# Kernel optimization log

Measured on AMD Instinct MI355X. Metric: run time of the kernel, lower is better.

## Reference

```python
import jax, jax.numpy as jnp
import numpy as np

L = 64        # label_size = len(label2id)
START = 62    # label2id['START']
STOP = 63     # label2id['STOP']
T = 200000    # sequence length
NEG = -10000.0


def setup_inputs() -> dict:
    key = jax.random.key(0)
    k1, k2 = jax.random.split(key)
    lstm_feats = jax.random.normal(k1, (1, T, L), dtype=jnp.float32)
    transitions = jax.random.normal(k2, (L, L), dtype=jnp.float32)
    # CRF constructor masks: cannot transition INTO START, cannot transition FROM STOP
    transitions = transitions.at[START, :].set(NEG).at[:, STOP].set(NEG)
    return {"lstm_feats": lstm_feats, "transitions": transitions}


def reference(lstm_feats, transitions):
    # Viterbi decode, vectorized over tags; lax.scan over time replaces the
    # nested Python loops of the original (same recurrence, same math).
    feats = lstm_feats[0]  # (T, L)
    init = jnp.full((L,), NEG, dtype=lstm_feats.dtype).at[START].set(0.0)

    def step(v, feat):
        # scores[next, prev] = v[prev] + transitions[next, prev]
        scores = v[None, :] + transitions          # (L, L)
        bp = jnp.argmax(scores, axis=1).astype(jnp.int32)  # backpointers per next_tag
        v_new = jnp.max(scores, axis=1) + feat     # viterbi vars + emission
        return v_new, bp

    v, bptrs = jax.lax.scan(step, init, feats)     # bptrs: (T, L)

    terminal = v + transitions[STOP]               # (L,)
    best = jnp.argmax(terminal).astype(jnp.int32)
    path_score = terminal[best]

    # Backtrack: reverse scan emits the tag chosen at each time step, in order.
    def back(tag, bp):
        return bp[tag], tag

    _, best_path = jax.lax.scan(back, best, bptrs, reverse=True)  # (T,) int32
    return path_score, best_path
```

## Files before the change

kernel.cpp:

```cpp
#include <hip/hip_runtime.h>

#define L 64
#define TLEN 200000
#define CH 528
#define NCH 379
#define LASTLEN (TLEN - (NCH - 1) * CH)
#define NEGV -10000.0f
#define STARTT 62
#define STOPT 63

#define CKPT_OFF 0
#define M_OFF ((NCH + 1) * L * 4)
#define ETAG_OFF (M_OFF + NCH * L)

typedef float f32x4 __attribute__((ext_vector_type(4)));

#define FAST_BARRIER() __asm__ volatile("s_barrier" ::: "memory")
#define STEP_BARRIER() __asm__ volatile("" ::: "memory")

__device__ __forceinline__ float max3f(float a, float b, float c) {
    float r;
    __asm__("v_max3_f32 %0, %1, %2, %3" : "=v"(r) : "v"(a), "v"(b), "v"(c));
    return r;
}

#define RL(v, k) __int_as_float(__builtin_amdgcn_readlane(__float_as_int(v), k))

__global__ __launch_bounds__(256, 1) void k_forward(const float* __restrict__ feats,
                                                    const float* __restrict__ trans,
                                                    float* __restrict__ ckpt) {
    const int tid = threadIdx.x;
    const int l = tid & 63;
    const int w = tid >> 6;
    const int n = l;
    const int pcol = 16 * w + (l & 15);
    const int wswz = (w + (n >> 2)) & 3;

    const f32x4* t4 = reinterpret_cast<const f32x4*>(trans) + n * 16 + w * 4;
    f32x4 q0 = t4[0], q1 = t4[1], q2 = t4[2], q3 = t4[3];
    __asm__ volatile("" : "+v"(q0), "+v"(q1), "+v"(q2), "+v"(q3));

    __shared__ __align__(16) float pm[2][L][4];

    float vcomb = (pcol == STARTT) ? 0.0f : NEGV;

    float fc[8];
#pragma unroll
    for (int j = 0; j < 8; ++j) fc[j] = feats[j * L + pcol];

    int nextck = 0, cidx = 0;

#define FWD_STEP(BUF, FEAT)                                                    \
    do {                                                                       \
                         \
        const float s0 = RL(vcomb, 0),  s1 = RL(vcomb, 1);                     \
        const float s2 = RL(vcomb, 2),  s3 = RL(vcomb, 3);                     \
        const float s4 = RL(vcomb, 4),  s5 = RL(vcomb, 5);                     \
        const float s6 = RL(vcomb, 6),  s7 = RL(vcomb, 7);                     \
        const float s8 = RL(vcomb, 8),  s9 = RL(vcomb, 9);                     \
        const float s10 = RL(vcomb, 10), s11 = RL(vcomb, 11);                  \
        const float s12 = RL(vcomb, 12), s13 = RL(vcomb, 13);                  \
        const float s14 = RL(vcomb, 14), s15 = RL(vcomb, 15);                  \
                     \
        const float c0 = s0 + q0.x,  c1 = s1 + q0.y;                           \
        const float c2 = s2 + q0.z,  c3 = s3 + q0.w;                           \
        const float c4 = s4 + q1.x,  c5 = s5 + q1.y;                           \
        const float c6 = s6 + q1.z,  c7 = s7 + q1.w;                           \
        const float c8 = s8 + q2.x,  c9 = s9 + q2.y;                           \
        const float c10 = s10 + q2.z, c11 = s11 + q2.w;                        \
        const float c12 = s12 + q3.x, c13 = s13 + q3.y;                        \
        const float c14 = s14 + q3.z, c15 = s15 + q3.w;                        \
        const float a0 = max3f(c0, c1, c2);                                    \
        const float a1 = max3f(c3, c4, c5);                                    \
        const float a2 = max3f(c6, c7, c8);                                    \
        const float a3 = max3f(c9, c10, c11);                                  \
        const float a4 = max3f(c12, c13, c14);                                 \
        const float pmv = fmaxf(max3f(a0, a1, a2), max3f(a3, a4, c15));        \
                                       \
        pm[BUF][n][wswz] = pmv;                                                \
        FAST_BARRIER();                                                        \
                       \
        const f32x4 pq = *reinterpret_cast<const f32x4*>(&pm[BUF][pcol][0]);   \
        vcomb = fmaxf(max3f(pq.x, pq.y, pq.z), pq.w) + (FEAT);                 \
    } while (0)

    for (int tb = 0; tb < TLEN; tb += 8) {
        if (tb == nextck) {
            if (l < 16) ckpt[cidx * L + 16 * w + l] = vcomb;
            nextck += CH;
            ++cidx;
        }
        float fn_[8];
        const bool more = (tb + 8) < TLEN;
        if (more) {
#pragma unroll
            for (int j = 0; j < 8; ++j) fn_[j] = feats[(tb + 8 + j) * L + pcol];
        }
        FWD_STEP(0, fc[0]);
        FWD_STEP(1, fc[1]);
        FWD_STEP(0, fc[2]);
        FWD_STEP(1, fc[3]);
        FWD_STEP(0, fc[4]);
        FWD_STEP(1, fc[5]);
        FWD_STEP(0, fc[6]);
        FWD_STEP(1, fc[7]);
        if (more) {
#pragma unroll
            for (int j = 0; j < 8; ++j) fc[j] = fn_[j];
        }
    }
    if (l < 16) ckpt[NCH * L + 16 * w + l] = vcomb;
#undef FWD_STEP
}

__device__ __forceinline__ void load_trow(const float* __restrict__ trans, int n, float* trow) {
#pragma unroll
    for (int i = 0; i < 16; ++i) {
        const f32x4 q = reinterpret_cast<const f32x4*>(trans)[n * 16 + i];
        trow[4 * i + 0] = q.x;
        trow[4 * i + 1] = q.y;
        trow[4 * i + 2] = q.z;
        trow[4 * i + 3] = q.w;
    }
}

__device__ __forceinline__ void replay_chunk(const float* __restrict__ feats,
                                             const float* __restrict__ ckpt,
                                             const float* trow, float* vsh,
                                             unsigned char* bpl, int c, int len, int n) {
    float vreg = ckpt[c * L + n];
    vsh[n] = vreg;
    STEP_BARRIER();
    const int base = c * CH;

    float fc[8];
#pragma unroll
    for (int j = 0; j < 8; ++j) fc[j] = feats[(base + j) * L + n];

    for (int sb = 0; sb < len; sb += 8) {
        float fn_[8];
        const bool more = (sb + 8) < len;
        if (more) {
#pragma unroll
            for (int j = 0; j < 8; ++j) fn_[j] = feats[(base + sb + 8 + j) * L + n];
        }
#pragma unroll
        for (int j = 0; j < 8; ++j) {
            float mc[4];
            int ic[4];
#pragma unroll
            for (int g = 0; g < 4; ++g) {
                float m = -INFINITY;
                int idx = g * 16;
#pragma unroll
                for (int r = 0; r < 4; ++r) {
                    const int pb = g * 16 + r * 4;
                    const f32x4 vv = *reinterpret_cast<const f32x4*>(vsh + pb);
                    const float a = vv.x + trow[pb + 0];
                    const float b = vv.y + trow[pb + 1];
                    const float cc = vv.z + trow[pb + 2];
                    const float d = vv.w + trow[pb + 3];
                    if (a > m)  { m = a;  idx = pb + 0; }
                    if (b > m)  { m = b;  idx = pb + 1; }
                    if (cc > m) { m = cc; idx = pb + 2; }
                    if (d > m)  { m = d;  idx = pb + 3; }
                }
                mc[g] = m;
                ic[g] = idx;
            }
            float m = mc[0];
            int idx = ic[0];
            if (mc[1] > m) { m = mc[1]; idx = ic[1]; }
            if (mc[2] > m) { m = mc[2]; idx = ic[2]; }
            if (mc[3] > m) { m = mc[3]; idx = ic[3]; }

            vreg = m + fc[j];
            bpl[(sb + j) * L + n] = (unsigned char)idx;
            vsh[n] = vreg;
            STEP_BARRIER();
        }
        if (more) {
#pragma unroll
            for (int j = 0; j < 8; ++j) fc[j] = fn_[j];
        }
    }
}

__global__ __launch_bounds__(64, 1) void k_maps(const float* __restrict__ feats,
                                                const float* __restrict__ trans,
                                                const float* __restrict__ ckpt,
                                                unsigned char* __restrict__ M) {
    const int c = blockIdx.x;
    const int n = threadIdx.x;
    const int len = (c == NCH - 1) ? LASTLEN : CH;

    __shared__ __align__(16) float vsh[L];
    __shared__ unsigned char bpl[CH * L];

    float trow[L];
    load_trow(trans, n, trow);
    replay_chunk(feats, ckpt, trow, vsh, bpl, c, len, n);
    __syncthreads();

    int tag = n;
    for (int s = len - 1; s >= 0; --s) tag = bpl[s * L + tag];
    M[c * L + n] = (unsigned char)tag;
}

__global__ __launch_bounds__(64, 1) void k_stitch(const float* __restrict__ trans,
                                                  const float* __restrict__ ckpt,
                                                  const unsigned char* __restrict__ M,
                                                  int* __restrict__ etag,
                                                  float* __restrict__ out) {
    const int n = threadIdx.x;
    __shared__ float tsh[L];
    __shared__ int bsh;
    __shared__ __align__(16) unsigned char msh[NCH * L];

    tsh[n] = ckpt[NCH * L + n] + trans[STOPT * L + n];
    __syncthreads();
    if (n == 0) {
        float m = tsh[0];
        int b = 0;
        for (int p = 1; p < L; ++p)
            if (tsh[p] > m) { m = tsh[p]; b = p; }
        out[0] = m;
        bsh = b;
    }
    __syncthreads();

    for (int i = n; i < (NCH * L) / 4; i += L)
        reinterpret_cast<int*>(msh)[i] = reinterpret_cast<const int*>(M)[i];
    __syncthreads();

    if (n == 0) {
        int carry = bsh;
        for (int c = NCH - 1; c >= 1; --c) {
            etag[c] = carry;
            carry = msh[c * L + carry];
        }
        etag[0] = carry;
    }
}

__global__ __launch_bounds__(64, 1) void k_emit(const float* __restrict__ feats,
                                                const float* __restrict__ trans,
                                                const float* __restrict__ ckpt,
                                                const int* __restrict__ etag,
                                                float* __restrict__ out) {
    const int c = blockIdx.x;
    const int n = threadIdx.x;
    const int len = (c == NCH - 1) ? LASTLEN : CH;

    __shared__ __align__(16) float vsh[L];
    __shared__ unsigned char bpl[CH * L];
    __shared__ unsigned char plc[CH];

    float trow[L];
    load_trow(trans, n, trow);
    replay_chunk(feats, ckpt, trow, vsh, bpl, c, len, n);
    __syncthreads();

    int tag = etag[c];
    for (int s = len - 1; s >= 0; --s) {
        if (n == 0) plc[s] = (unsigned char)tag;
        tag = bpl[s * L + tag];
    }
    __syncthreads();

    for (int i = n; i < len; i += L)
        out[1 + c * CH + i] = (float)plc[i];
}

extern "C" void kernel_launch(void* const* d_in, const int* in_sizes, int n_in,
                              void* d_out, int out_size, void* d_ws, size_t ws_size,
                              hipStream_t stream) {
    const float* feats = (const float*)d_in[0];
    const float* trans = (const float*)d_in[1];
    float* out = (float*)d_out;
    char* ws = (char*)d_ws;
    float* ckpt = (float*)(ws + CKPT_OFF);
    unsigned char* M = (unsigned char*)(ws + M_OFF);
    int* etag = (int*)(ws + ETAG_OFF);

    hipLaunchKernelGGL(k_forward, dim3(1), dim3(256), 0, stream, feats, trans, ckpt);
    hipLaunchKernelGGL(k_maps, dim3(NCH), dim3(64), 0, stream, feats, trans, ckpt, M);
    hipLaunchKernelGGL(k_stitch, dim3(1), dim3(64), 0, stream, trans, ckpt, M, etag, out);
    hipLaunchKernelGGL(k_emit, dim3(NCH), dim3(64), 0, stream, feats, trans, ckpt, etag, out);
}
```

Before: 36.67 ms.

## Repartition forward Viterbi step: quad lanes per tag with LDS broadcast and DPP reduction

Each forward step used to pull 16 previous scores out of the wave with scalar readlanes, reduce partial maxima, exchange the partials through LDS and finish the reduction after the barrier. Now each quad of lanes owns one next-tag and reads the previous score vector from a double-buffered LDS array with vector loads. It reduces its 16-column slices, combines the quad with two DPP permutes, and writes the new score back before the barrier. This removes the serialized readlane chain from the per-step critical path. In exchange it adds wide LDS reads and DPP hazards on every step, and keeps a barrier with no explicit wait after the LDS write.

```diff
diff --git a/kernel.cpp b/kernel.cpp
--- a/kernel.cpp
+++ b/kernel.cpp
@@ -15,6 +15,7 @@
 
 typedef float f32x4 __attribute__((ext_vector_type(4)));
 
+#define WAVE_BARRIER() __asm__ volatile("s_waitcnt lgkmcnt(0)\ns_barrier" ::: "memory")
 #define FAST_BARRIER() __asm__ volatile("s_barrier" ::: "memory")
 #define STEP_BARRIER() __asm__ volatile("" ::: "memory")
 
@@ -24,7 +25,9 @@
     return r;
 }
 
-#define RL(v, k) __int_as_float(__builtin_amdgcn_readlane(__float_as_int(v), k))
+#define QPERM(x, ctrl)                                                         \
+    __int_as_float(__builtin_amdgcn_update_dpp(                                \
+        __float_as_int(x), __float_as_int(x), ctrl, 0xf, 0xf, false))
 
 __global__ __launch_bounds__(256, 1) void k_forward(const float* __restrict__ feats,
                                                     const float* __restrict__ trans,
@@ -32,61 +35,48 @@
     const int tid = threadIdx.x;
     const int l = tid & 63;
     const int w = tid >> 6;
-    const int n = l;
-    const int pcol = 16 * w + (l & 15);
-    const int wswz = (w + (n >> 2)) & 3;
-
-    const f32x4* t4 = reinterpret_cast<const f32x4*>(trans) + n * 16 + w * 4;
+    const int d = 16 * w + (l >> 2);
+    const int g = l & 3;
+    const bool writer = (g == 0);
+
+    const f32x4* t4 = reinterpret_cast<const f32x4*>(trans) + d * 16 + g * 4;
     f32x4 q0 = t4[0], q1 = t4[1], q2 = t4[2], q3 = t4[3];
     __asm__ volatile("" : "+v"(q0), "+v"(q1), "+v"(q2), "+v"(q3));
 
-    __shared__ __align__(16) float pm[2][L][4];
-
-    float vcomb = (pcol == STARTT) ? 0.0f : NEGV;
+    __shared__ __align__(16) float vbuf[2][L];
+
+    float vq = (d == STARTT) ? 0.0f : NEGV;
+    if (writer) vbuf[0][d] = vq;
+    WAVE_BARRIER();
 
     float fc[8];
 #pragma unroll
-    for (int j = 0; j < 8; ++j) fc[j] = feats[j * L + pcol];
+    for (int j = 0; j < 8; ++j) fc[j] = feats[j * L + d];
 
     int nextck = 0, cidx = 0;
 
-#define FWD_STEP(BUF, FEAT)                                                    \
+#define FWD_STEP(RD, WR, FEAT)                                                 \
     do {                                                                       \
-                         \
-        const float s0 = RL(vcomb, 0),  s1 = RL(vcomb, 1);                     \
-        const float s2 = RL(vcomb, 2),  s3 = RL(vcomb, 3);                     \
-        const float s4 = RL(vcomb, 4),  s5 = RL(vcomb, 5);                     \
-        const float s6 = RL(vcomb, 6),  s7 = RL(vcomb, 7);                     \
-        const float s8 = RL(vcomb, 8),  s9 = RL(vcomb, 9);                     \
-        const float s10 = RL(vcomb, 10), s11 = RL(vcomb, 11);                  \
-        const float s12 = RL(vcomb, 12), s13 = RL(vcomb, 13);                  \
-        const float s14 = RL(vcomb, 14), s15 = RL(vcomb, 15);                  \
-                     \
-        const float c0 = s0 + q0.x,  c1 = s1 + q0.y;                           \
-        const float c2 = s2 + q0.z,  c3 = s3 + q0.w;                           \
-        const float c4 = s4 + q1.x,  c5 = s5 + q1.y;                           \
-        const float c6 = s6 + q1.z,  c7 = s7 + q1.w;                           \
-        const float c8 = s8 + q2.x,  c9 = s9 + q2.y;                           \
-        const float c10 = s10 + q2.z, c11 = s11 + q2.w;                        \
-        const float c12 = s12 + q3.x, c13 = s13 + q3.y;                        \
-        const float c14 = s14 + q3.z, c15 = s15 + q3.w;                        \
-        const float a0 = max3f(c0, c1, c2);                                    \
-        const float a1 = max3f(c3, c4, c5);                                    \
-        const float a2 = max3f(c6, c7, c8);                                    \
-        const float a3 = max3f(c9, c10, c11);                                  \
-        const float a4 = max3f(c12, c13, c14);                                 \
-        const float pmv = fmaxf(max3f(a0, a1, a2), max3f(a3, a4, c15));        \
-                                       \
-        pm[BUF][n][wswz] = pmv;                                                \
+        const f32x4 va0 = *reinterpret_cast<const f32x4*>(&vbuf[RD][16 * g + 0]);  \
+        const f32x4 va1 = *reinterpret_cast<const f32x4*>(&vbuf[RD][16 * g + 4]);  \
+        const f32x4 va2 = *reinterpret_cast<const f32x4*>(&vbuf[RD][16 * g + 8]);  \
+        const f32x4 va3 = *reinterpret_cast<const f32x4*>(&vbuf[RD][16 * g + 12]); \
+        const f32x4 s0 = va0 + q0, s1 = va1 + q1, s2 = va2 + q2, s3 = va3 + q3;    \
+        const float m0 = max3f(fmaxf(s0.x, s0.y), s0.z, s0.w);                 \
+        const float m1 = max3f(fmaxf(s1.x, s1.y), s1.z, s1.w);                 \
+        const float m2 = max3f(fmaxf(s2.x, s2.y), s2.z, s2.w);                 \
+        const float m3 = max3f(fmaxf(s3.x, s3.y), s3.z, s3.w);                 \
+        float x = fmaxf(max3f(m0, m1, m2), m3);                                \
+        x = fmaxf(x, QPERM(x, 0xB1));                                          \
+        x = fmaxf(x, QPERM(x, 0x4E));                                          \
+        vq = x + (FEAT);                                                       \
+        if (writer) vbuf[WR][d] = vq;                                          \
         FAST_BARRIER();                                                        \
-                       \
-        const f32x4 pq = *reinterpret_cast<const f32x4*>(&pm[BUF][pcol][0]);   \
-        vcomb = fmaxf(max3f(pq.x, pq.y, pq.z), pq.w) + (FEAT);                 \
     } while (0)
 
     for (int tb = 0; tb < TLEN; tb += 8) {
         if (tb == nextck) {
-            if (l < 16) ckpt[cidx * L + 16 * w + l] = vcomb;
+            if (writer) ckpt[cidx * L + d] = vq;
             nextck += CH;
             ++cidx;
         }
@@ -94,22 +84,22 @@
         const bool more = (tb + 8) < TLEN;
         if (more) {
 #pragma unroll
-            for (int j = 0; j < 8; ++j) fn_[j] = feats[(tb + 8 + j) * L + pcol];
-        }
-        FWD_STEP(0, fc[0]);
-        FWD_STEP(1, fc[1]);
-        FWD_STEP(0, fc[2]);
-        FWD_STEP(1, fc[3]);
-        FWD_STEP(0, fc[4]);
-        FWD_STEP(1, fc[5]);
-        FWD_STEP(0, fc[6]);
-        FWD_STEP(1, fc[7]);
+            for (int j = 0; j < 8; ++j) fn_[j] = feats[(tb + 8 + j) * L + d];
+        }
+        FWD_STEP(0, 1, fc[0]);
+        FWD_STEP(1, 0, fc[1]);
+        FWD_STEP(0, 1, fc[2]);
+        FWD_STEP(1, 0, fc[3]);
+        FWD_STEP(0, 1, fc[4]);
+        FWD_STEP(1, 0, fc[5]);
+        FWD_STEP(0, 1, fc[6]);
+        FWD_STEP(1, 0, fc[7]);
         if (more) {
 #pragma unroll
             for (int j = 0; j < 8; ++j) fc[j] = fn_[j];
         }
     }
-    if (l < 16) ckpt[NCH * L + 16 * w + l] = vcomb;
+    if (writer) ckpt[NCH * L + d] = vq;
 #undef FWD_STEP
 }
 
```

After: 35.32 ms. 1.04x faster.
